# Performance work log

Measured on AMD Instinct MI355X. Metric: run time of the kernel, lower is better.

## Reference

```python
import jax, jax.numpy as jnp
import numpy as np

B, N, F, R, DEG, STEPS = 4, 1024, 128, 16, 16, 2


def setup_inputs() -> dict:
    key = jax.random.key(0)
    ks = jax.random.split(key, 12)
    BN = B * N
    E = BN * DEG

    def edges(k):
        # edges kept within each graph of size N, then offset per graph
        e = jax.random.randint(k, (2, E), 0, N)
        off = jnp.repeat(jnp.arange(B, dtype=jnp.int32) * N, N * DEG)
        return e + off[None, :]

    return {
        "x_s": jax.random.normal(ks[0], (BN, F), jnp.float32),
        "edge_index_s": edges(ks[1]),
        "x_t": jax.random.normal(ks[2], (BN, F), jnp.float32),
        "edge_index_t": edges(ks[3]),
        "W1_self": jax.random.normal(ks[4], (F, F), jnp.float32) / np.float32(np.sqrt(F)),
        "W1_nbr": jax.random.normal(ks[5], (F, F), jnp.float32) / np.float32(np.sqrt(F)),
        "b1": jnp.zeros((F,), jnp.float32),
        "W2_self": jax.random.normal(ks[6], (R, R), jnp.float32) / np.float32(np.sqrt(R)),
        "W2_nbr": jax.random.normal(ks[7], (R, R), jnp.float32) / np.float32(np.sqrt(R)),
        "b2": jnp.zeros((R,), jnp.float32),
        "Wm1": jax.random.normal(ks[8], (R, R), jnp.float32) / np.float32(np.sqrt(R)),
        "bm1": jnp.zeros((R,), jnp.float32),
        "Wm2": jax.random.normal(ks[9], (R, 1), jnp.float32) / np.float32(np.sqrt(R)),
        "bm2": jnp.zeros((1,), jnp.float32),
        "r_steps": jax.random.normal(ks[10], (STEPS, B, N, R), jnp.float32),
    }


def _psi(x, ei, Ws, Wn, b):
    # simple GraphConv: self transform + summed neighbor transform
    agg = jax.ops.segment_sum(x[ei[0]], ei[1], num_segments=x.shape[0])
    return jax.nn.relu(x @ Ws + agg @ Wn + b)


def reference(x_s, edge_index_s, x_t, edge_index_t, W1_self, W1_nbr, b1,
              W2_self, W2_nbr, b2, Wm1, bm1, Wm2, bm2, r_steps):
    # psi_1 on both graphs, then dense-batch to [B, N, F] (equal-size graphs,
    # so masks are all-True and masked_softmax == softmax)
    h_s = _psi(x_s, edge_index_s, W1_self, W1_nbr, b1).reshape(B, N, F)
    h_t = _psi(x_t, edge_index_t, W1_self, W1_nbr, b1).reshape(B, N, F)

    S_hat = jnp.einsum('bsf,btf->bst', h_s, h_t)  # [B, Ns, Nt]
    S_0 = jax.nn.softmax(S_hat, axis=-1)

    for i in range(STEPS):
        S = jax.nn.softmax(S_hat, axis=-1)
        r_s = r_steps[i]                             # [B, N, R]
        r_t = jnp.einsum('bst,bsr->btr', S, r_s)     # S^T @ r_s
        o_s = _psi(r_s.reshape(B * N, R), edge_index_s, W2_self, W2_nbr, b2).reshape(B, N, R)
        o_t = _psi(r_t.reshape(B * N, R), edge_index_t, W2_self, W2_nbr, b2).reshape(B, N, R)
        D = o_s[:, :, None, :] - o_t[:, None, :, :]  # [B, Ns, Nt, R]
        upd = (jax.nn.relu(D @ Wm1 + bm1) @ Wm2 + bm2)[..., 0]
        S_hat = S_hat + upd

    S_L = jax.nn.softmax(S_hat, axis=-1)
    return (S_0, S_L)
```

## Files before the change

### kernel.cpp

```cpp
#include <hip/hip_runtime.h>

#define B_ 4
#define N_ 1024
#define F_ 128
#define R_ 16
#define E_ 65536
#define BN_ 4096

__global__ __launch_bounds__(256) void hist_k(
    const int* __restrict__ eis, const int* __restrict__ eit, int* __restrict__ counts) {
  const int* ei = blockIdx.y ? eit : eis;
  int* c = counts + blockIdx.y * BN_;
  int e = blockIdx.x * 256 + threadIdx.x;
  atomicAdd(c + ei[E_ + e], 1);
}

__global__ __launch_bounds__(256) void csr_scan(
    const int* __restrict__ counts, int* __restrict__ offs, int* __restrict__ cursor) {
  const int* c = counts + blockIdx.x * BN_;
  int* o = offs + blockIdx.x * (BN_ + 1);
  int* cur = cursor + blockIdx.x * BN_;
  int tid = threadIdx.x;
  int base = tid * 16;
  int local[16], sum = 0;
#pragma unroll
  for (int i = 0; i < 16; i++) { local[i] = sum; sum += c[base + i]; }
  __shared__ int csum[256];
  csum[tid] = sum;
  __syncthreads();
  for (int d = 1; d < 256; d <<= 1) {
    int v = (tid >= d) ? csum[tid - d] : 0;
    __syncthreads();
    csum[tid] += v;
    __syncthreads();
  }
  int prev = (tid == 0) ? 0 : csum[tid - 1];
#pragma unroll
  for (int i = 0; i < 16; i++) { int off = prev + local[i]; o[base + i] = off; cur[base + i] = off; }
  if (tid == 255) o[BN_] = csum[255];
}

__global__ __launch_bounds__(256) void csr_fill(
    const int* __restrict__ eis, const int* __restrict__ eit,
    int* __restrict__ cursor, int* __restrict__ csr) {
  const int* ei = blockIdx.y ? eit : eis;
  int* cur = cursor + blockIdx.y * BN_;
  int* cs = csr + blockIdx.y * E_;
  int e = blockIdx.x * 256 + threadIdx.x;
  int src = ei[e], dst = ei[E_ + e];
  int pos = atomicAdd(cur + dst, 1);
  cs[pos] = src;
}

__global__ __launch_bounds__(256) void gather_f(
    const float* __restrict__ xs, const float* __restrict__ xt,
    const int* __restrict__ csr, const int* __restrict__ offs,
    float* __restrict__ aggs, float* __restrict__ aggt) {
  const float* x = blockIdx.y ? xt : xs;
  const int* cs = csr + blockIdx.y * E_;
  const int* of = offs + blockIdx.y * (BN_ + 1);
  float* agg = blockIdx.y ? aggt : aggs;
  int node = blockIdx.x * 2 + (threadIdx.x >> 7);
  int ch = threadIdx.x & 127;
  int j0 = of[node], j1 = of[node + 1];
  float acc = 0.f, acc2 = 0.f;
  int j = j0;
  for (; j + 1 < j1; j += 2) {
    int s0 = cs[j], s1 = cs[j + 1];
    acc  += x[(size_t)s0 * F_ + ch];
    acc2 += x[(size_t)s1 * F_ + ch];
  }
  if (j < j1) acc += x[(size_t)cs[j] * F_ + ch];
  agg[(size_t)node * F_ + ch] = acc + acc2;
}

__global__ __launch_bounds__(256) void gather_r(
    const float* __restrict__ rs, const float* __restrict__ rtv,
    const int* __restrict__ csr, const int* __restrict__ offs,
    float* __restrict__ aggs, float* __restrict__ aggt) {
  const float* v = blockIdx.y ? rtv : rs;
  const int* cs = csr + blockIdx.y * E_;
  const int* of = offs + blockIdx.y * (BN_ + 1);
  float* agg = blockIdx.y ? aggt : aggs;
  int node = blockIdx.x * 16 + (threadIdx.x >> 4);
  int ch = threadIdx.x & 15;
  int j0 = of[node], j1 = of[node + 1];
  float acc = 0.f, acc2 = 0.f;
  int j = j0;
  for (; j + 1 < j1; j += 2) {
    int s0 = cs[j], s1 = cs[j + 1];
    acc  += v[(size_t)s0 * R_ + ch];
    acc2 += v[(size_t)s1 * R_ + ch];
  }
  if (j < j1) acc += v[(size_t)cs[j] * R_ + ch];
  agg[(size_t)node * R_ + ch] = acc + acc2;
}

__global__ __launch_bounds__(256) void psi1_gemm(
    const float* __restrict__ xs, const float* __restrict__ aggs,
    const float* __restrict__ xt, const float* __restrict__ aggt,
    const float* __restrict__ Ws, const float* __restrict__ Wn,
    const float* __restrict__ bias, float* __restrict__ hs, float* __restrict__ ht) {
  const float* x   = blockIdx.z ? xt   : xs;
  const float* agg = blockIdx.z ? aggt : aggs;
  float*       h   = blockIdx.z ? ht   : hs;
  int n0 = blockIdx.x * 64, m0 = blockIdx.y * 64;
  int tid = threadIdx.x, tx = tid & 15, ty = tid >> 4;
  __shared__ __align__(16) float sA[16][68];
  __shared__ __align__(16) float sB[16][68];
  float acc[4][4] = {};
  for (int phase = 0; phase < 2; phase++) {
    const float* A  = phase ? agg : x;
    const float* Bw = phase ? Wn  : Ws;
    for (int kb = 0; kb < F_; kb += 16) {
      int row = tid >> 2, k4 = (tid & 3) * 4;
      float4 va = *(const float4*)(A + (size_t)(m0 + row) * F_ + kb + k4);
      sA[k4 + 0][row] = va.x; sA[k4 + 1][row] = va.y;
      sA[k4 + 2][row] = va.z; sA[k4 + 3][row] = va.w;
      int k = tid >> 4, n4 = (tid & 15) * 4;
      *(float4*)&sB[k][n4] = *(const float4*)(Bw + (size_t)(kb + k) * F_ + n0 + n4);
      __syncthreads();
#pragma unroll
      for (int kk = 0; kk < 16; kk++) {
        float a[4], bb[4];
        *(float4*)a  = *(const float4*)&sA[kk][ty * 4];
        *(float4*)bb = *(const float4*)&sB[kk][tx * 4];
#pragma unroll
        for (int i = 0; i < 4; i++)
#pragma unroll
          for (int j = 0; j < 4; j++) acc[i][j] += a[i] * bb[j];
      }
      __syncthreads();
    }
  }
  float4 bv = *(const float4*)(bias + n0 + tx * 4);
  float bj[4] = {bv.x, bv.y, bv.z, bv.w};
#pragma unroll
  for (int i = 0; i < 4; i++) {
    int m = m0 + ty * 4 + i;
    float4 o;
    o.x = fmaxf(acc[i][0] + bj[0], 0.f); o.y = fmaxf(acc[i][1] + bj[1], 0.f);
    o.z = fmaxf(acc[i][2] + bj[2], 0.f); o.w = fmaxf(acc[i][3] + bj[3], 0.f);
    *(float4*)(h + (size_t)m * F_ + n0 + tx * 4) = o;
  }
}

__global__ __launch_bounds__(256) void shat_gemm(
    const float* __restrict__ hs, const float* __restrict__ ht, float* __restrict__ S) {
  int b = blockIdx.z;
  int n0 = blockIdx.x * 128, m0 = blockIdx.y * 128;
  int tid = threadIdx.x, tx = tid & 15, ty = tid >> 4;
  __shared__ __align__(16) float sA[16][132];
  __shared__ __align__(16) float sB[16][132];
  float acc[8][8] = {};
  const float* Ag = hs + (size_t)(b * N_ + m0) * F_;
  const float* Bg = ht + (size_t)(b * N_ + n0) * F_;
  for (int kb = 0; kb < F_; kb += 16) {
#pragma unroll
    for (int l = 0; l < 2; l++) {
      int idx = tid + l * 256;
      int row = idx >> 2, k4 = (idx & 3) * 4;
      float4 va = *(const float4*)(Ag + (size_t)row * F_ + kb + k4);
      sA[k4 + 0][row] = va.x; sA[k4 + 1][row] = va.y;
      sA[k4 + 2][row] = va.z; sA[k4 + 3][row] = va.w;
      float4 vb = *(const float4*)(Bg + (size_t)row * F_ + kb + k4);
      sB[k4 + 0][row] = vb.x; sB[k4 + 1][row] = vb.y;
      sB[k4 + 2][row] = vb.z; sB[k4 + 3][row] = vb.w;
    }
    __syncthreads();
#pragma unroll
    for (int kk = 0; kk < 16; kk++) {
      float a[8], bb[8];
      *(float4*)&a[0]  = *(const float4*)&sA[kk][ty * 8];
      *(float4*)&a[4]  = *(const float4*)&sA[kk][ty * 8 + 4];
      *(float4*)&bb[0] = *(const float4*)&sB[kk][tx * 8];
      *(float4*)&bb[4] = *(const float4*)&sB[kk][tx * 8 + 4];
#pragma unroll
      for (int i = 0; i < 8; i++)
#pragma unroll
        for (int j = 0; j < 8; j++) acc[i][j] += a[i] * bb[j];
    }
    __syncthreads();
  }
#pragma unroll
  for (int i = 0; i < 8; i++) {
    size_t off = ((size_t)(b * N_ + m0 + ty * 8 + i)) * N_ + n0 + tx * 8;
    float4 o0 = {acc[i][0], acc[i][1], acc[i][2], acc[i][3]};
    float4 o1 = {acc[i][4], acc[i][5], acc[i][6], acc[i][7]};
    *(float4*)(S + off) = o0; *(float4*)(S + off + 4) = o1;
  }
}

__global__ __launch_bounds__(256) void softmax_row(
    const float* __restrict__ in, float* __restrict__ out) {
  int row = blockIdx.x;
  float4 v = ((const float4*)(in + (size_t)row * N_))[threadIdx.x];
  float m = fmaxf(fmaxf(v.x, v.y), fmaxf(v.z, v.w));
#pragma unroll
  for (int o = 32; o > 0; o >>= 1) m = fmaxf(m, __shfl_down(m, o, 64));
  __shared__ float rmax[4], rsum[4];
  int wave = threadIdx.x >> 6, lane = threadIdx.x & 63;
  if (lane == 0) rmax[wave] = m;
  __syncthreads();
  m = fmaxf(fmaxf(rmax[0], rmax[1]), fmaxf(rmax[2], rmax[3]));
  float e0 = __expf(v.x - m), e1 = __expf(v.y - m);
  float e2 = __expf(v.z - m), e3 = __expf(v.w - m);
  float s = e0 + e1 + e2 + e3;
#pragma unroll
  for (int o = 32; o > 0; o >>= 1) s += __shfl_down(s, o, 64);
  if (lane == 0) rsum[wave] = s;
  __syncthreads();
  s = rsum[0] + rsum[1] + rsum[2] + rsum[3];
  float inv = 1.f / s;
  float4 o4 = {e0 * inv, e1 * inv, e2 * inv, e3 * inv};
  ((float4*)(out + (size_t)row * N_))[threadIdx.x] = o4;
}

__global__ __launch_bounds__(256) void rt_part(
    const float* __restrict__ S, const float* __restrict__ rs, float* __restrict__ part) {
  int b = blockIdx.z, c = blockIdx.y, t0 = blockIdx.x * 256;
  int tid = threadIdx.x;
  int s0 = c * 32;
  __shared__ float rsh[32][16];
  if (tid < 128) {
    int srow = tid >> 2, c4 = (tid & 3) * 4;
    float4 v = *(const float4*)(rs + ((size_t)(b * N_ + s0 + srow)) * R_ + c4);
    rsh[srow][c4] = v.x; rsh[srow][c4 + 1] = v.y;
    rsh[srow][c4 + 2] = v.z; rsh[srow][c4 + 3] = v.w;
  }
  __syncthreads();
  float acc[16] = {};
  const float* Sp = S + ((size_t)(b * N_ + s0)) * N_ + t0 + tid;
#pragma unroll
  for (int s = 0; s < 32; s++) {
    float sv = Sp[(size_t)s * N_];
#pragma unroll
    for (int r = 0; r < 16; r++) acc[r] += sv * rsh[s][r];
  }
  float* o = part + ((size_t)((b * 32 + c) * N_) + t0 + tid) * R_;
  *(float4*)(o + 0)  = *(float4*)&acc[0];
  *(float4*)(o + 4)  = *(float4*)&acc[4];
  *(float4*)(o + 8)  = *(float4*)&acc[8];
  *(float4*)(o + 12) = *(float4*)&acc[12];
}

__global__ __launch_bounds__(256) void rt_reduce(
    const float* __restrict__ part, float* __restrict__ rt) {
  int gid = blockIdx.x * 256 + threadIdx.x;
  int b = gid >> 12, tr = gid & 4095;
  const float* p = part + (size_t)b * (32 * N_ * R_) + (size_t)tr * 4;
  float4 acc = {0.f, 0.f, 0.f, 0.f};
#pragma unroll
  for (int c = 0; c < 32; c++) {
    float4 v = *(const float4*)(p + (size_t)c * (N_ * R_));
    acc.x += v.x; acc.y += v.y; acc.z += v.z; acc.w += v.w;
  }
  ((float4*)rt)[gid] = acc;
}

__global__ __launch_bounds__(256) void psi2p(
    const float* __restrict__ vs, const float* __restrict__ aggs_,
    const float* __restrict__ vt, const float* __restrict__ aggt_,
    const float* __restrict__ W2s, const float* __restrict__ W2n,
    const float* __restrict__ b2, const float* __restrict__ Wm1,
    float* __restrict__ Ps, float* __restrict__ Pt) {
  const float* v   = blockIdx.y ? vt    : vs;
  const float* agg = blockIdx.y ? aggt_ : aggs_;
  float*       P   = blockIdx.y ? Pt    : Ps;
  int col = threadIdx.x & 15, row = threadIdx.x >> 4;
  int r0 = blockIdx.x * 16;
  __shared__ float sWs[16][16], sWn[16][16], sWm[16][17];
  __shared__ float sv[16][17], sa[16][17], so[16][17];
  sWs[row][col] = W2s[row * 16 + col];
  sWn[row][col] = W2n[row * 16 + col];
  sWm[row][col] = Wm1[row * 16 + col];
  sv[row][col] = v[(size_t)(r0 + row) * R_ + col];
  sa[row][col] = agg[(size_t)(r0 + row) * R_ + col];
  __syncthreads();
  float o = b2[col];
#pragma unroll
  for (int k = 0; k < 16; k++) o += sv[row][k] * sWs[k][col] + sa[row][k] * sWn[k][col];
  so[row][col] = fmaxf(o, 0.f);
  __syncthreads();
  float p = 0;
#pragma unroll
  for (int k = 0; k < 16; k++) p += so[row][k] * sWm[k][col];
  P[(size_t)(r0 + row) * R_ + col] = p;
}

__global__ __launch_bounds__(256) void upd_kernel(
    float* __restrict__ Shat, const float* __restrict__ Ps, const float* __restrict__ Pt,
    const float* __restrict__ bm1, const float* __restrict__ Wm2,
    const float* __restrict__ bm2) {
  int b = blockIdx.z, s0 = blockIdx.y * 4, t0 = blockIdx.x * 256;
  int tid = threadIdx.x;
  __shared__ float pt[256][17];
  __shared__ float ps[4][16];
  __shared__ float sb[16], sw[16];
  for (int i = tid; i < 1024; i += 256) {
    int tr = i >> 2, c = (i & 3) * 4;
    const float4 v = *(const float4*)(Pt + ((size_t)(b * N_ + t0 + tr)) * R_ + c);
    pt[tr][c] = v.x; pt[tr][c + 1] = v.y; pt[tr][c + 2] = v.z; pt[tr][c + 3] = v.w;
  }
  if (tid < 64) ps[tid >> 4][tid & 15] = Ps[((size_t)(b * N_ + s0 + (tid >> 4))) * R_ + (tid & 15)];
  if (tid < 16) { sb[tid] = bm1[tid]; sw[tid] = Wm2[tid]; }
  __syncthreads();
  float bm2v = bm2[0];
  float ptl[16];
#pragma unroll
  for (int r = 0; r < 16; r++) ptl[r] = pt[tid][r];
#pragma unroll
  for (int si = 0; si < 4; si++) {
    size_t off = ((size_t)(b * N_ + s0 + si)) * N_ + t0 + tid;
    float sum = bm2v;
#pragma unroll
    for (int r = 0; r < 16; r++) sum += fmaxf(ps[si][r] - ptl[r] + sb[r], 0.f) * sw[r];
    Shat[off] += sum;
  }
}

extern "C" void kernel_launch(void* const* d_in, const int* in_sizes, int n_in,
                              void* d_out, int out_size, void* d_ws, size_t ws_size,
                              hipStream_t stream) {
  const float* x_s = (const float*)d_in[0];
  const int*   ei_s = (const int*)d_in[1];
  const float* x_t = (const float*)d_in[2];
  const int*   ei_t = (const int*)d_in[3];
  const float* W1s = (const float*)d_in[4];
  const float* W1n = (const float*)d_in[5];
  const float* b1  = (const float*)d_in[6];
  const float* W2s = (const float*)d_in[7];
  const float* W2n = (const float*)d_in[8];
  const float* b2  = (const float*)d_in[9];
  const float* Wm1 = (const float*)d_in[10];
  const float* bm1 = (const float*)d_in[11];
  const float* Wm2 = (const float*)d_in[12];
  const float* bm2 = (const float*)d_in[13];
  const float* r_steps = (const float*)d_in[14];

  float* out = (float*)d_out;
  float* S0 = out;
  float* SL = out + (size_t)B_ * N_ * N_;

  float* ws = (float*)d_ws;
  float* agg_s = ws;
  float* agg_t = ws + 524288;
  float* h_s   = ws + 1048576;
  float* h_t   = ws + 1572864;
  float* part  = ws;
  float* Shat  = ws + 2097152;
  float* rtb   = ws + 6291456;
  float* agg2s = ws + 6356992;
  float* agg2t = ws + 6422528;
  float* Ps    = ws + 6488064;
  float* Pt    = ws + 6553600;
  int* counts  = (int*)(ws + 6619136);
  int* cursor  = (int*)(ws + 6627328);
  int* offs    = (int*)(ws + 6635520);
  int* csr     = (int*)(ws + 6643720);

  hipMemsetAsync(counts, 0, 2 * BN_ * sizeof(int), stream);
  hist_k<<<dim3(E_ / 256, 2), 256, 0, stream>>>(ei_s, ei_t, counts);
  csr_scan<<<2, 256, 0, stream>>>(counts, offs, cursor);
  csr_fill<<<dim3(E_ / 256, 2), 256, 0, stream>>>(ei_s, ei_t, cursor, csr);

  gather_f<<<dim3(BN_ / 2, 2), 256, 0, stream>>>(x_s, x_t, csr, offs, agg_s, agg_t);
  psi1_gemm<<<dim3(2, 64, 2), 256, 0, stream>>>(x_s, agg_s, x_t, agg_t, W1s, W1n, b1, h_s, h_t);

  shat_gemm<<<dim3(8, 8, 4), 256, 0, stream>>>(h_s, h_t, Shat);
  softmax_row<<<B_ * N_, 256, 0, stream>>>(Shat, S0);

  for (int step = 0; step < 2; step++) {
    const float* rs = r_steps + (size_t)step * B_ * N_ * R_;
    const float* Scur;
    if (step == 0) {
      Scur = S0;
    } else {
      softmax_row<<<B_ * N_, 256, 0, stream>>>(Shat, SL);
      Scur = SL;
    }
    rt_part<<<dim3(4, 32, 4), 256, 0, stream>>>(Scur, rs, part);
    rt_reduce<<<64, 256, 0, stream>>>(part, rtb);
    gather_r<<<dim3(BN_ / 16, 2), 256, 0, stream>>>(rs, rtb, csr, offs, agg2s, agg2t);
    psi2p<<<dim3(256, 2), 256, 0, stream>>>(rs, agg2s, rtb, agg2t, W2s, W2n, b2, Wm1, Ps, Pt);
    upd_kernel<<<dim3(4, 256, 4), 256, 0, stream>>>(Shat, Ps, Pt, bm1, Wm2, bm2);
  }

  softmax_row<<<B_ * N_, 256, 0, stream>>>(Shat, SL);
}
```

Baseline: 268.7 us.

## Fuse R-gather into psi2, compute softmax stats instead of materializing S in step

In the second refinement step, the softmax of S_hat is no longer written out in full. A small row_stats kernel computes per-row max and inverse sum, and rt_part applies exp and normalisation on the fly while reading S_hat. This removes one full 16M-float write and read. The neighbour aggregation for the R-dim features is fused into the psi2 kernel, dropping the gather_r launch and its intermediate buffers, and the gather loops are unrolled to 4 accumulators. The exponentials are now computed inside the reduction loop, which adds ALU work there.

```diff
diff --git a/kernel.cpp b/kernel.cpp
--- a/kernel.cpp
+++ b/kernel.cpp
@@ -63,37 +63,17 @@
   int node = blockIdx.x * 2 + (threadIdx.x >> 7);
   int ch = threadIdx.x & 127;
   int j0 = of[node], j1 = of[node + 1];
-  float acc = 0.f, acc2 = 0.f;
+  float a0 = 0.f, a1 = 0.f, a2 = 0.f, a3 = 0.f;
   int j = j0;
-  for (; j + 1 < j1; j += 2) {
-    int s0 = cs[j], s1 = cs[j + 1];
-    acc  += x[(size_t)s0 * F_ + ch];
-    acc2 += x[(size_t)s1 * F_ + ch];
-  }
-  if (j < j1) acc += x[(size_t)cs[j] * F_ + ch];
-  agg[(size_t)node * F_ + ch] = acc + acc2;
-}
-
-__global__ __launch_bounds__(256) void gather_r(
-    const float* __restrict__ rs, const float* __restrict__ rtv,
-    const int* __restrict__ csr, const int* __restrict__ offs,
-    float* __restrict__ aggs, float* __restrict__ aggt) {
-  const float* v = blockIdx.y ? rtv : rs;
-  const int* cs = csr + blockIdx.y * E_;
-  const int* of = offs + blockIdx.y * (BN_ + 1);
-  float* agg = blockIdx.y ? aggt : aggs;
-  int node = blockIdx.x * 16 + (threadIdx.x >> 4);
-  int ch = threadIdx.x & 15;
-  int j0 = of[node], j1 = of[node + 1];
-  float acc = 0.f, acc2 = 0.f;
-  int j = j0;
-  for (; j + 1 < j1; j += 2) {
-    int s0 = cs[j], s1 = cs[j + 1];
-    acc  += v[(size_t)s0 * R_ + ch];
-    acc2 += v[(size_t)s1 * R_ + ch];
-  }
-  if (j < j1) acc += v[(size_t)cs[j] * R_ + ch];
-  agg[(size_t)node * R_ + ch] = acc + acc2;
+  for (; j + 3 < j1; j += 4) {
+    int s0 = cs[j], s1 = cs[j + 1], s2 = cs[j + 2], s3 = cs[j + 3];
+    a0 += x[(size_t)s0 * F_ + ch];
+    a1 += x[(size_t)s1 * F_ + ch];
+    a2 += x[(size_t)s2 * F_ + ch];
+    a3 += x[(size_t)s3 * F_ + ch];
+  }
+  for (; j < j1; j++) a0 += x[(size_t)cs[j] * F_ + ch];
+  agg[(size_t)node * F_ + ch] = (a0 + a1) + (a2 + a3);
 }
 
 __global__ __launch_bounds__(256) void psi1_gemm(
@@ -216,17 +196,45 @@
   ((float4*)(out + (size_t)row * N_))[threadIdx.x] = o4;
 }
 
-__global__ __launch_bounds__(256) void rt_part(
-    const float* __restrict__ S, const float* __restrict__ rs, float* __restrict__ part) {
+__global__ __launch_bounds__(256) void row_stats(
+    const float* __restrict__ in, float2* __restrict__ stats) {
+  int row = blockIdx.x;
+  float4 v = ((const float4*)(in + (size_t)row * N_))[threadIdx.x];
+  float m = fmaxf(fmaxf(v.x, v.y), fmaxf(v.z, v.w));
+#pragma unroll
+  for (int o = 32; o > 0; o >>= 1) m = fmaxf(m, __shfl_down(m, o, 64));
+  __shared__ float rmax[4], rsum[4];
+  int wave = threadIdx.x >> 6, lane = threadIdx.x & 63;
+  if (lane == 0) rmax[wave] = m;
+  __syncthreads();
+  m = fmaxf(fmaxf(rmax[0], rmax[1]), fmaxf(rmax[2], rmax[3]));
+  float s = __expf(v.x - m) + __expf(v.y - m) + __expf(v.z - m) + __expf(v.w - m);
+#pragma unroll
+  for (int o = 32; o > 0; o >>= 1) s += __shfl_down(s, o, 64);
+  if (lane == 0) rsum[wave] = s;
+  __syncthreads();
+  if (threadIdx.x == 0) {
+    float tot = rsum[0] + rsum[1] + rsum[2] + rsum[3];
+    stats[row] = make_float2(m, 1.f / tot);
+  }
+}
+
+template <bool EXP>
+__global__ __launch_bounds__(256) void rt_part_k(
+    const float* __restrict__ S, const float2* __restrict__ stats,
+    const float* __restrict__ rs, float* __restrict__ part) {
   int b = blockIdx.z, c = blockIdx.y, t0 = blockIdx.x * 256;
   int tid = threadIdx.x;
   int s0 = c * 32;
   __shared__ float rsh[32][16];
+  __shared__ float sstat[64];
   if (tid < 128) {
     int srow = tid >> 2, c4 = (tid & 3) * 4;
     float4 v = *(const float4*)(rs + ((size_t)(b * N_ + s0 + srow)) * R_ + c4);
     rsh[srow][c4] = v.x; rsh[srow][c4 + 1] = v.y;
     rsh[srow][c4 + 2] = v.z; rsh[srow][c4 + 3] = v.w;
+  } else if (EXP && tid < 192) {
+    sstat[tid - 128] = ((const float*)(stats + b * N_ + s0))[tid - 128];
   }
   __syncthreads();
   float acc[16] = {};
@@ -234,6 +242,7 @@
 #pragma unroll
   for (int s = 0; s < 32; s++) {
     float sv = Sp[(size_t)s * N_];
+    if (EXP) sv = __expf(sv - sstat[2 * s]) * sstat[2 * s + 1];
 #pragma unroll
     for (int r = 0; r < 16; r++) acc[r] += sv * rsh[s][r];
   }
@@ -258,24 +267,36 @@
   ((float4*)rt)[gid] = acc;
 }
 
-__global__ __launch_bounds__(256) void psi2p(
-    const float* __restrict__ vs, const float* __restrict__ aggs_,
-    const float* __restrict__ vt, const float* __restrict__ aggt_,
+__global__ __launch_bounds__(256) void gpsi2p(
+    const float* __restrict__ vs, const float* __restrict__ vt,
+    const int* __restrict__ csr, const int* __restrict__ offs,
     const float* __restrict__ W2s, const float* __restrict__ W2n,
     const float* __restrict__ b2, const float* __restrict__ Wm1,
     float* __restrict__ Ps, float* __restrict__ Pt) {
-  const float* v   = blockIdx.y ? vt    : vs;
-  const float* agg = blockIdx.y ? aggt_ : aggs_;
-  float*       P   = blockIdx.y ? Pt    : Ps;
+  const float* v = blockIdx.y ? vt : vs;
+  const int* cs = csr + blockIdx.y * E_;
+  const int* of = offs + blockIdx.y * (BN_ + 1);
+  float* P = blockIdx.y ? Pt : Ps;
   int col = threadIdx.x & 15, row = threadIdx.x >> 4;
-  int r0 = blockIdx.x * 16;
+  int node = blockIdx.x * 16 + row;
+  int j0 = of[node], j1 = of[node + 1];
+  float a0 = 0.f, a1 = 0.f, a2 = 0.f, a3 = 0.f;
+  int j = j0;
+  for (; j + 3 < j1; j += 4) {
+    int s0 = cs[j], s1 = cs[j + 1], s2 = cs[j + 2], s3 = cs[j + 3];
+    a0 += v[(size_t)s0 * R_ + col];
+    a1 += v[(size_t)s1 * R_ + col];
+    a2 += v[(size_t)s2 * R_ + col];
+    a3 += v[(size_t)s3 * R_ + col];
+  }
+  for (; j < j1; j++) a0 += v[(size_t)cs[j] * R_ + col];
   __shared__ float sWs[16][16], sWn[16][16], sWm[16][17];
   __shared__ float sv[16][17], sa[16][17], so[16][17];
   sWs[row][col] = W2s[row * 16 + col];
   sWn[row][col] = W2n[row * 16 + col];
   sWm[row][col] = Wm1[row * 16 + col];
-  sv[row][col] = v[(size_t)(r0 + row) * R_ + col];
-  sa[row][col] = agg[(size_t)(r0 + row) * R_ + col];
+  sv[row][col] = v[(size_t)node * R_ + col];
+  sa[row][col] = (a0 + a1) + (a2 + a3);
   __syncthreads();
   float o = b2[col];
 #pragma unroll
@@ -285,7 +306,7 @@
   float p = 0;
 #pragma unroll
   for (int k = 0; k < 16; k++) p += so[row][k] * sWm[k][col];
-  P[(size_t)(r0 + row) * R_ + col] = p;
+  P[(size_t)node * R_ + col] = p;
 }
 
 __global__ __launch_bounds__(256) void upd_kernel(
@@ -350,8 +371,7 @@
   float* part  = ws;
   float* Shat  = ws + 2097152;
   float* rtb   = ws + 6291456;
-  float* agg2s = ws + 6356992;
-  float* agg2t = ws + 6422528;
+  float2* stats = (float2*)(ws + 6356992);
   float* Ps    = ws + 6488064;
   float* Pt    = ws + 6553600;
   int* counts  = (int*)(ws + 6619136);
@@ -372,17 +392,14 @@
 
   for (int step = 0; step < 2; step++) {
     const float* rs = r_steps + (size_t)step * B_ * N_ * R_;
-    const float* Scur;
     if (step == 0) {
-      Scur = S0;
+      rt_part_k<false><<<dim3(4, 32, 4), 256, 0, stream>>>(S0, nullptr, rs, part);
     } else {
-      softmax_row<<<B_ * N_, 256, 0, stream>>>(Shat, SL);
-      Scur = SL;
+      row_stats<<<B_ * N_, 256, 0, stream>>>(Shat, stats);
+      rt_part_k<true><<<dim3(4, 32, 4), 256, 0, stream>>>(Shat, stats, rs, part);
     }
-    rt_part<<<dim3(4, 32, 4), 256, 0, stream>>>(Scur, rs, part);
     rt_reduce<<<64, 256, 0, stream>>>(part, rtb);
-    gather_r<<<dim3(BN_ / 16, 2), 256, 0, stream>>>(rs, rtb, csr, offs, agg2s, agg2t);
-    psi2p<<<dim3(256, 2), 256, 0, stream>>>(rs, agg2s, rtb, agg2t, W2s, W2n, b2, Wm1, Ps, Pt);
+    gpsi2p<<<dim3(256, 2), 256, 0, stream>>>(rs, rtb, csr, offs, W2s, W2n, b2, Wm1, Ps, Pt);
     upd_kernel<<<dim3(4, 256, 4), 256, 0, stream>>>(Shat, Ps, Pt, bm1, Wm2, bm2);
   }
 
```

Result: faster. 257.0 us (-4.3%).
